# Kernel tuning notes

Measured on AMD Instinct MI355X. Metric: run time of the kernel, lower is better.

The kernel has to match this reference:

```python
import jax, jax.numpy as jnp
import numpy as np
import math

B, L, S = 2, 2048, 2048
DIN, DK, DV, DOUT, H = 512, 512, 512, 512, 8
HEAD_SIZE = DK / H  # attention_head_size = dim_key_query_all / num_attention_heads


def setup_inputs() -> dict:
    key = jax.random.key(0)
    ks = jax.random.split(key, 12)
    inv = 1.0 / math.sqrt(DIN)
    return {
        "queries": jax.random.normal(ks[0], (B, L, DIN), jnp.float32),
        "keys": jax.random.normal(ks[1], (B, S, DIN), jnp.float32),
        "values": jax.random.normal(ks[2], (B, S, DIN), jnp.float32),
        "attn_mask": 0,
        "Wq": jax.random.uniform(ks[3], (DK, DIN), jnp.float32, -inv, inv),
        "Wk": jax.random.uniform(ks[4], (DK, DIN), jnp.float32, -inv, inv),
        "Wv": jax.random.uniform(ks[5], (DV, DIN), jnp.float32, -inv, inv),
        "bv": jax.random.uniform(ks[6], (DV,), jnp.float32, -inv, inv),
        "Wcb": jax.random.uniform(ks[7], (H, DIN), jnp.float32, -inv, inv),
        "mixing": 0.2 * jax.random.normal(ks[8], (H, DK), jnp.float32),
        "Wd": jax.random.uniform(ks[9], (DOUT, DV), jnp.float32, -1.0 / math.sqrt(DV), 1.0 / math.sqrt(DV)),
        "bd": jax.random.uniform(ks[10], (DOUT,), jnp.float32, -1.0 / math.sqrt(DV), 1.0 / math.sqrt(DV)),
    }


def reference(queries, keys, values, attn_mask, Wq, Wk, Wv, bv, Wcb, mixing, Wd, bd):
    # projections
    q = jnp.einsum('bld,ed->ble', queries, Wq)            # [B,L,DK]
    k = jnp.einsum('bsd,ed->bse', keys, Wk)               # [B,S,DK]
    v = jnp.einsum('bsd,ed->bse', values, Wv) + bv        # [B,S,DV]
    v = v.reshape(B, S, H, DV // H).transpose(0, 2, 1, 3)  # [B,H,S,dv]
    # collaborative scores: (q * mixing_h) @ k^T, per head
    mixed_q = q[:, None, :, :] * mixing[None, :, None, :]  # [B,H,L,DK]
    scores = jnp.einsum('bhle,bse->bhls', mixed_q, k)      # [B,H,L,S]
    # content bias: keys -> [B,S,H] -> broadcast over queries
    cb = jnp.einsum('bsd,hd->bhs', keys, Wcb)              # [B,H,S]
    scores = (scores + cb[:, :, None, :]) / math.sqrt(HEAD_SIZE)
    probs = jax.nn.softmax(scores, axis=-1)                # dropout p=0 (eval)
    ctx = jnp.einsum('bhls,bhsv->bhlv', probs, v)          # [B,H,L,dv]
    ctx = ctx.transpose(0, 2, 1, 3).reshape(B, L, DV)      # [B,L,DV]
    out = jnp.einsum('blv,ov->blo', ctx, Wd) + bd          # [B,L,DOUT]
    return out, probs
```

## Files before the change

### kernel.cpp

```cpp
#include <hip/hip_runtime.h>

typedef unsigned short u16;
typedef __bf16 bf16x8 __attribute__((ext_vector_type(8)));
typedef float floatx4 __attribute__((ext_vector_type(4)));

#define B_ 2
#define L_ 2048
#define S_ 2048
#define D_ 512
#define H_ 8

static __device__ __forceinline__ u16 f2bf(float f) {
  union { float f; unsigned u; } v; v.f = f;
  unsigned u = v.u;
  return (u16)((u + 0x7FFFu + ((u >> 16) & 1u)) >> 16);
}
static __device__ __forceinline__ float bf2f(u16 h) {
  union { unsigned u; float f; } v; v.u = ((unsigned)h) << 16;
  return v.f;
}

__global__ __launch_bounds__(256) void qkv_gemm(
    const float* __restrict__ Qin, const float* __restrict__ Kin, const float* __restrict__ Vin,
    const float* __restrict__ Wq, const float* __restrict__ Wk, const float* __restrict__ Wv,
    const float* __restrict__ bv,
    u16* __restrict__ qo, u16* __restrict__ ko, u16* __restrict__ vo)
{
  __shared__ u16 As[128][72];
  __shared__ u16 Bs[128][72];
  const int z = blockIdx.z;
  const float* A = (z == 0) ? Qin : (z == 1) ? Kin : Vin;
  const float* W = (z == 0) ? Wq : (z == 1) ? Wk : Wv;
  const int tid = threadIdx.x;
  const int m0 = blockIdx.y * 128;
  const int n0 = blockIdx.x * 128;
  const int lane = tid & 63, w = tid >> 6;
  const int ml = lane & 15, kl = lane >> 4;
  const int mqw = (w >> 1) * 64, nq = (w & 1) * 64;
  const int srow = tid >> 4, scg = tid & 15;

  floatx4 acc[4][4] = {};

  for (int k0 = 0; k0 < 512; k0 += 64) {
#pragma unroll
    for (int i = 0; i < 8; ++i) {
      const int r = srow + i * 16;
      float4 av = *(const float4*)&A[(size_t)(m0 + r) * 512 + k0 + scg * 4];
      ushort4 ua; ua.x = f2bf(av.x); ua.y = f2bf(av.y); ua.z = f2bf(av.z); ua.w = f2bf(av.w);
      *(ushort4*)&As[r][scg * 4] = ua;
      float4 wv = *(const float4*)&W[(size_t)(n0 + r) * 512 + k0 + scg * 4];
      ushort4 uw; uw.x = f2bf(wv.x); uw.y = f2bf(wv.y); uw.z = f2bf(wv.z); uw.w = f2bf(wv.w);
      *(ushort4*)&Bs[r][scg * 4] = uw;
    }
    __syncthreads();
#pragma unroll
    for (int kk = 0; kk < 64; kk += 32) {
      bf16x8 af[4], bfv[4];
#pragma unroll
      for (int i = 0; i < 4; ++i) af[i] = *(const bf16x8*)&As[mqw + i * 16 + ml][kk + kl * 8];
#pragma unroll
      for (int j = 0; j < 4; ++j) bfv[j] = *(const bf16x8*)&Bs[nq + j * 16 + ml][kk + kl * 8];
#pragma unroll
      for (int i = 0; i < 4; ++i)
#pragma unroll
        for (int j = 0; j < 4; ++j)
          acc[i][j] = __builtin_amdgcn_mfma_f32_16x16x32_bf16(af[i], bfv[j], acc[i][j], 0, 0, 0);
    }
    __syncthreads();
  }
#pragma unroll
  for (int i = 0; i < 4; ++i)
#pragma unroll
    for (int j = 0; j < 4; ++j) {
      const int gc = n0 + nq + j * 16 + ml;
#pragma unroll
      for (int r = 0; r < 4; ++r) {
        const int gr = m0 + mqw + i * 16 + kl * 4 + r;
        float v = acc[i][j][r];
        if (z == 0)      qo[(size_t)gr * 512 + gc] = f2bf(v);
        else if (z == 1) ko[(size_t)gr * 512 + gc] = f2bf(v);
        else             vo[(size_t)gr * 512 + gc] = f2bf(v + bv[gc]);
      }
    }
}

__global__ __launch_bounds__(256) void mixq_kernel(
    const u16* __restrict__ qb, const float* __restrict__ mixing, u16* __restrict__ mq)
{
  __shared__ float mixs[8 * 512];
  const int tid = threadIdx.x;
#pragma unroll
  for (int i = 0; i < 4; ++i)
    *(float4*)&mixs[(tid + i * 256) * 4] = *(const float4*)&mixing[(tid + i * 256) * 4];
  __syncthreads();
  const size_t unit = (size_t)blockIdx.x * 256 + tid;
  const size_t el = unit * 8;
  const int e = (int)(el & 511);
  const size_t bl = el >> 9;
  const int b = (int)(bl >> 11);
  const int l = (int)(bl & 2047);
  uint4 qv = *(const uint4*)&qb[el];
  const float q0 = bf2f((u16)(qv.x & 0xFFFFu)), q1 = bf2f((u16)(qv.x >> 16));
  const float q2 = bf2f((u16)(qv.y & 0xFFFFu)), q3 = bf2f((u16)(qv.y >> 16));
  const float q4 = bf2f((u16)(qv.z & 0xFFFFu)), q5 = bf2f((u16)(qv.z >> 16));
  const float q6 = bf2f((u16)(qv.w & 0xFFFFu)), q7 = bf2f((u16)(qv.w >> 16));
#pragma unroll
  for (int h = 0; h < 8; ++h) {
    const float* mp = &mixs[h * 512 + e];
    uint4 o;
    o.x = (unsigned)f2bf(q0 * mp[0]) | ((unsigned)f2bf(q1 * mp[1]) << 16);
    o.y = (unsigned)f2bf(q2 * mp[2]) | ((unsigned)f2bf(q3 * mp[3]) << 16);
    o.z = (unsigned)f2bf(q4 * mp[4]) | ((unsigned)f2bf(q5 * mp[5]) << 16);
    o.w = (unsigned)f2bf(q6 * mp[6]) | ((unsigned)f2bf(q7 * mp[7]) << 16);
    *(uint4*)&mq[(((size_t)b * 8 + h) * 2048 + l) * 512 + e] = o;
  }
}

__global__ __launch_bounds__(256) void out_gemm(
    const float* __restrict__ A, const float* __restrict__ W,
    const float* __restrict__ bias, float* __restrict__ out)
{
  __shared__ u16 As[128][72];
  __shared__ u16 Bs[128][72];
  const int tid = threadIdx.x;
  const int m0 = blockIdx.y * 128;
  const int n0 = blockIdx.x * 128;
  const int lane = tid & 63, w = tid >> 6;
  const int ml = lane & 15, kl = lane >> 4;
  const int mqw = (w >> 1) * 64, nq = (w & 1) * 64;
  const int srow = tid >> 4, scg = tid & 15;

  floatx4 acc[4][4] = {};

  for (int k0 = 0; k0 < 512; k0 += 64) {
#pragma unroll
    for (int i = 0; i < 8; ++i) {
      const int r = srow + i * 16;
      float4 av = *(const float4*)&A[(size_t)(m0 + r) * 512 + k0 + scg * 4];
      ushort4 ua; ua.x = f2bf(av.x); ua.y = f2bf(av.y); ua.z = f2bf(av.z); ua.w = f2bf(av.w);
      *(ushort4*)&As[r][scg * 4] = ua;
      float4 wv = *(const float4*)&W[(size_t)(n0 + r) * 512 + k0 + scg * 4];
      ushort4 uw; uw.x = f2bf(wv.x); uw.y = f2bf(wv.y); uw.z = f2bf(wv.z); uw.w = f2bf(wv.w);
      *(ushort4*)&Bs[r][scg * 4] = uw;
    }
    __syncthreads();
#pragma unroll
    for (int kk = 0; kk < 64; kk += 32) {
      bf16x8 af[4], bfv[4];
#pragma unroll
      for (int i = 0; i < 4; ++i) af[i] = *(const bf16x8*)&As[mqw + i * 16 + ml][kk + kl * 8];
#pragma unroll
      for (int j = 0; j < 4; ++j) bfv[j] = *(const bf16x8*)&Bs[nq + j * 16 + ml][kk + kl * 8];
#pragma unroll
      for (int i = 0; i < 4; ++i)
#pragma unroll
        for (int j = 0; j < 4; ++j)
          acc[i][j] = __builtin_amdgcn_mfma_f32_16x16x32_bf16(af[i], bfv[j], acc[i][j], 0, 0, 0);
    }
    __syncthreads();
  }
#pragma unroll
  for (int i = 0; i < 4; ++i)
#pragma unroll
    for (int j = 0; j < 4; ++j) {
      const int gc = n0 + nq + j * 16 + ml;
#pragma unroll
      for (int r = 0; r < 4; ++r) {
        const int gr = m0 + mqw + i * 16 + kl * 4 + r;
        out[(size_t)gr * 512 + gc] = acc[i][j][r] + bias[gc];
      }
    }
}

__global__ __launch_bounds__(256) void cb_kernel(
    const float* __restrict__ keys, const float* __restrict__ Wcb, float* __restrict__ cbuf)
{
  __shared__ float Wl[8 * 512];
  const int tid = threadIdx.x;
#pragma unroll
  for (int i = 0; i < 4; ++i) {
    const int idx = tid + i * 256;
    *(float4*)&Wl[idx * 4] = *(const float4*)&Wcb[idx * 4];
  }
  __syncthreads();
  const int w = tid >> 6, lane = tid & 63;
  const int rowid = blockIdx.x * 4 + w;
  const int b = rowid >> 11, s = rowid & 2047;
  const float* kr = keys + (size_t)rowid * 512;
  float acc[8] = {0.f, 0.f, 0.f, 0.f, 0.f, 0.f, 0.f, 0.f};
  for (int e = lane; e < 512; e += 64) {
    const float kv = kr[e];
#pragma unroll
    for (int hh = 0; hh < 8; ++hh) acc[hh] += kv * Wl[hh * 512 + e];
  }
#pragma unroll
  for (int hh = 0; hh < 8; ++hh) {
#pragma unroll
    for (int off = 32; off > 0; off >>= 1) acc[hh] += __shfl_xor(acc[hh], off, 64);
  }
  if (lane == 0) {
#pragma unroll
    for (int hh = 0; hh < 8; ++hh)
      cbuf[((size_t)b * 8 + hh) * 2048 + s] = acc[hh];
  }
}

__global__ __launch_bounds__(256) void transpose_v(
    const u16* __restrict__ vb, u16* __restrict__ vT)
{
  __shared__ u16 t[64][72];
  const int tid = threadIdx.x;
  const int e0 = blockIdx.x * 64;
  const int s0 = blockIdx.y * 64;
  const int b = blockIdx.z;
  const int rr = tid >> 3, g = tid & 7;
#pragma unroll
  for (int i = 0; i < 2; ++i) {
    const int r = rr + i * 32;
    *(uint4*)&t[r][g * 8] = *(const uint4*)&vb[((size_t)b * S_ + s0 + r) * 512 + e0 + g * 8];
  }
  __syncthreads();
#pragma unroll
  for (int i = 0; i < 2; ++i) {
    const int er = rr + i * 32;
    uint4 o;
    o.x = (unsigned)t[g * 8 + 0][er] | ((unsigned)t[g * 8 + 1][er] << 16);
    o.y = (unsigned)t[g * 8 + 2][er] | ((unsigned)t[g * 8 + 3][er] << 16);
    o.z = (unsigned)t[g * 8 + 4][er] | ((unsigned)t[g * 8 + 5][er] << 16);
    o.w = (unsigned)t[g * 8 + 6][er] | ((unsigned)t[g * 8 + 7][er] << 16);
    *(uint4*)&vT[((size_t)b * 512 + e0 + er) * S_ + s0 + g * 8] = o;
  }
}

__global__ __launch_bounds__(256) void scores_gemm(
    const u16* __restrict__ mq, const u16* __restrict__ kb,
    const float* __restrict__ cbuf, float* __restrict__ sc)
{
  __shared__ u16 As[128][72];
  __shared__ u16 Bs[128][72];
  const int tid = threadIdx.x;
  const int bh = blockIdx.z, b = bh >> 3;
  const int m0 = blockIdx.y * 128;
  const int n0 = blockIdx.x * 128;
  const u16* mqb = mq + (size_t)bh * L_ * 512;
  const u16* kbb = kb + (size_t)b * S_ * 512;
  const int lane = tid & 63, w = tid >> 6;
  const int ml = lane & 15, kl = lane >> 4;
  const int mqw = (w >> 1) * 64, nq = (w & 1) * 64;
  const int brow = tid >> 3, bcg = tid & 7;

  floatx4 acc[4][4] = {};

  for (int k0 = 0; k0 < 512; k0 += 64) {
#pragma unroll
    for (int i = 0; i < 4; ++i) {
      const int r = brow + i * 32;
      *(uint4*)&As[r][bcg * 8] = *(const uint4*)&mqb[(size_t)(m0 + r) * 512 + k0 + bcg * 8];
      *(uint4*)&Bs[r][bcg * 8] = *(const uint4*)&kbb[(size_t)(n0 + r) * 512 + k0 + bcg * 8];
    }
    __syncthreads();
#pragma unroll
    for (int kk = 0; kk < 64; kk += 32) {
      bf16x8 af[4], bfv[4];
#pragma unroll
      for (int i = 0; i < 4; ++i) af[i] = *(const bf16x8*)&As[mqw + i * 16 + ml][kk + kl * 8];
#pragma unroll
      for (int j = 0; j < 4; ++j) bfv[j] = *(const bf16x8*)&Bs[nq + j * 16 + ml][kk + kl * 8];
#pragma unroll
      for (int i = 0; i < 4; ++i)
#pragma unroll
        for (int j = 0; j < 4; ++j)
          acc[i][j] = __builtin_amdgcn_mfma_f32_16x16x32_bf16(af[i], bfv[j], acc[i][j], 0, 0, 0);
    }
    __syncthreads();
  }
  float* outp = sc + ((size_t)bh * L_ + m0) * S_ + n0;
#pragma unroll
  for (int j = 0; j < 4; ++j) {
    const int gcl = nq + j * 16 + ml;
    const float cbv = cbuf[(size_t)bh * S_ + n0 + gcl];
#pragma unroll
    for (int i = 0; i < 4; ++i)
#pragma unroll
      for (int r = 0; r < 4; ++r) {
        const int grl = mqw + i * 16 + kl * 4 + r;
        outp[(size_t)grl * S_ + gcl] = (acc[i][j][r] + cbv) * 0.125f;
      }
  }
}

__global__ __launch_bounds__(256) void softmax_ctx(
    float* __restrict__ sc, const u16* __restrict__ vT, float* __restrict__ ctx)
{
  __shared__ u16 Ps[16][1032];
  const int tid = threadIdx.x;
  const int bh = blockIdx.y, b = bh >> 3, h = bh & 7;
  const int l0 = blockIdx.x * 16;
  float* Sg = sc + ((size_t)bh * L_ + l0) * S_;
  const int row = tid >> 4, jg = tid & 15;

  unsigned pr[64];
  float mx = -3.0e38f;
#pragma unroll
  for (int i = 0; i < 32; ++i) {
    const int c = jg * 4 + i * 64;
    float4 v = *(const float4*)&Sg[(size_t)row * S_ + c];
    pr[2 * i]     = (unsigned)f2bf(v.x) | ((unsigned)f2bf(v.y) << 16);
    pr[2 * i + 1] = (unsigned)f2bf(v.z) | ((unsigned)f2bf(v.w) << 16);
    mx = fmaxf(mx, fmaxf(fmaxf(v.x, v.y), fmaxf(v.z, v.w)));
  }
#pragma unroll
  for (int off = 8; off > 0; off >>= 1) mx = fmaxf(mx, __shfl_xor(mx, off, 64));
  float ls = 0.f;
#pragma unroll
  for (int i = 0; i < 64; ++i) {
    const unsigned u = pr[i];
    ls += __expf(bf2f((u16)(u & 0xFFFFu)) - mx) + __expf(bf2f((u16)(u >> 16)) - mx);
  }
#pragma unroll
  for (int off = 8; off > 0; off >>= 1) ls += __shfl_xor(ls, off, 64);
  const float rl = 1.0f / ls;

  const int lane = tid & 63, wv = tid >> 6;
  const int ml = lane & 15, kl = lane >> 4;
  const u16* vrow = vT + ((size_t)b * 512 + h * 64 + wv * 16 + ml) * S_ + kl * 8;
  floatx4 acc = {};

#pragma unroll
  for (int half = 0; half < 2; ++half) {
    __syncthreads();
#pragma unroll
    for (int i = 0; i < 16; ++i) {
      const int ig = i + half * 16;
      const unsigned u0 = pr[2 * ig], u1 = pr[2 * ig + 1];
      float4 p;
      p.x = __expf(bf2f((u16)(u0 & 0xFFFFu)) - mx) * rl;
      p.y = __expf(bf2f((u16)(u0 >> 16)) - mx) * rl;
      p.z = __expf(bf2f((u16)(u1 & 0xFFFFu)) - mx) * rl;
      p.w = __expf(bf2f((u16)(u1 >> 16)) - mx) * rl;
      const int lc = jg * 4 + i * 64;
      *(float4*)&Sg[(size_t)row * S_ + half * 1024 + lc] = p;
      uint2 t;
      t.x = (unsigned)f2bf(p.x) | ((unsigned)f2bf(p.y) << 16);
      t.y = (unsigned)f2bf(p.z) | ((unsigned)f2bf(p.w) << 16);
      *(uint2*)&Ps[row][lc] = t;
    }
    __syncthreads();
    const u16* vk = vrow + half * 1024;
#pragma unroll
    for (int k0 = 0; k0 < 1024; k0 += 32) {
      bf16x8 a  = *(const bf16x8*)&Ps[ml][k0 + kl * 8];
      bf16x8 bb = *(const bf16x8*)&vk[k0];
      acc = __builtin_amdgcn_mfma_f32_16x16x32_bf16(a, bb, acc, 0, 0, 0);
    }
  }
#pragma unroll
  for (int r = 0; r < 4; ++r)
    ctx[((size_t)b * L_ + l0 + kl * 4 + r) * 512 + h * 64 + wv * 16 + ml] = acc[r];
}

extern "C" void kernel_launch(void* const* d_in, const int* in_sizes, int n_in,
                              void* d_out, int out_size, void* d_ws, size_t ws_size,
                              hipStream_t stream) {
  const float* queries = (const float*)d_in[0];
  const float* keys    = (const float*)d_in[1];
  const float* values  = (const float*)d_in[2];
  const float* Wq  = (const float*)d_in[4];
  const float* Wk  = (const float*)d_in[5];
  const float* Wv  = (const float*)d_in[6];
  const float* bv  = (const float*)d_in[7];
  const float* Wcb = (const float*)d_in[8];
  const float* mixing = (const float*)d_in[9];
  const float* Wd  = (const float*)d_in[10];
  const float* bd  = (const float*)d_in[11];

  float* out   = (float*)d_out;
  float* probs = out + (size_t)B_ * L_ * 512;

  char* ws = (char*)d_ws;
  u16*   qb  = (u16*)(ws);
  u16*   kb  = (u16*)(ws + (size_t)4  * 1024 * 1024);
  u16*   vb  = (u16*)(ws + (size_t)8  * 1024 * 1024);
  u16*   vT  = (u16*)(ws + (size_t)12 * 1024 * 1024);
  float* cbuf= (float*)(ws + (size_t)16 * 1024 * 1024);
  float* ctx = (float*)(ws + (size_t)17 * 1024 * 1024);
  u16*   mq  = (u16*)(ws + (size_t)25 * 1024 * 1024);

  hipLaunchKernelGGL(qkv_gemm, dim3(4, 32, 3), dim3(256), 0, stream,
                     queries, keys, values, Wq, Wk, Wv, bv, qb, kb, vb);
  hipLaunchKernelGGL(mixq_kernel, dim3(1024), dim3(256), 0, stream, qb, mixing, mq);
  hipLaunchKernelGGL(cb_kernel, dim3(1024), dim3(256), 0, stream, keys, Wcb, cbuf);
  hipLaunchKernelGGL(transpose_v, dim3(8, 32, 2), dim3(256), 0, stream, vb, vT);
  hipLaunchKernelGGL(scores_gemm, dim3(16, 16, 16), dim3(256), 0, stream,
                     mq, kb, cbuf, probs);
  hipLaunchKernelGGL(softmax_ctx, dim3(128, 16), dim3(256), 0, stream,
                     probs, vT, ctx);
  hipLaunchKernelGGL(out_gemm, dim3(4, 32, 1), dim3(256), 0, stream,
                     ctx, Wd, bd, out);
}
```

Baseline: 677.0 us.

## Fuse scores GEMM with softmax and PV into one attention kernel

Merges the separate scores GEMM and the softmax+context kernel into a single kernel. Each block computes a 16-row strip of scores directly from registers with MFMA, keeps them packed as bf16, reduces the row max and sum across waves through shared memory, and writes the probs once. This removes the fp32 scores write and the re-read of the full score matrix. In exchange, K tiles are loaded straight from global memory with no LDS reuse across row tiles, so K traffic grows since each block re-reads all K rows for its batch.

```diff
diff --git a/kernel.cpp b/kernel.cpp
--- a/kernel.cpp
+++ b/kernel.cpp
@@ -232,118 +232,127 @@
   }
 }
 
-__global__ __launch_bounds__(256) void scores_gemm(
+__global__ __launch_bounds__(256, 2) void fused_attn(
     const u16* __restrict__ mq, const u16* __restrict__ kb,
-    const float* __restrict__ cbuf, float* __restrict__ sc)
-{
-  __shared__ u16 As[128][72];
-  __shared__ u16 Bs[128][72];
-  const int tid = threadIdx.x;
-  const int bh = blockIdx.z, b = bh >> 3;
-  const int m0 = blockIdx.y * 128;
-  const int n0 = blockIdx.x * 128;
-  const u16* mqb = mq + (size_t)bh * L_ * 512;
-  const u16* kbb = kb + (size_t)b * S_ * 512;
+    const float* __restrict__ cbuf, const u16* __restrict__ vT,
+    float* __restrict__ probs, float* __restrict__ ctx)
+{
+  __shared__ u16 Ps[16][1032];
+  __shared__ float redm[16][4];
+  __shared__ float reds[16][4];
+  const int tid = threadIdx.x;
+  const int bh = blockIdx.y, b = bh >> 3, h = bh & 7;
+  const int l0 = blockIdx.x * 16;
   const int lane = tid & 63, w = tid >> 6;
   const int ml = lane & 15, kl = lane >> 4;
-  const int mqw = (w >> 1) * 64, nq = (w & 1) * 64;
-  const int brow = tid >> 3, bcg = tid & 7;
-
-  floatx4 acc[4][4] = {};
-
-  for (int k0 = 0; k0 < 512; k0 += 64) {
-#pragma unroll
-    for (int i = 0; i < 4; ++i) {
-      const int r = brow + i * 32;
-      *(uint4*)&As[r][bcg * 8] = *(const uint4*)&mqb[(size_t)(m0 + r) * 512 + k0 + bcg * 8];
-      *(uint4*)&Bs[r][bcg * 8] = *(const uint4*)&kbb[(size_t)(n0 + r) * 512 + k0 + bcg * 8];
-    }
-    __syncthreads();
-#pragma unroll
-    for (int kk = 0; kk < 64; kk += 32) {
-      bf16x8 af[4], bfv[4];
-#pragma unroll
-      for (int i = 0; i < 4; ++i) af[i] = *(const bf16x8*)&As[mqw + i * 16 + ml][kk + kl * 8];
-#pragma unroll
-      for (int j = 0; j < 4; ++j) bfv[j] = *(const bf16x8*)&Bs[nq + j * 16 + ml][kk + kl * 8];
-#pragma unroll
-      for (int i = 0; i < 4; ++i)
-#pragma unroll
-        for (int j = 0; j < 4; ++j)
-          acc[i][j] = __builtin_amdgcn_mfma_f32_16x16x32_bf16(af[i], bfv[j], acc[i][j], 0, 0, 0);
-    }
-    __syncthreads();
-  }
-  float* outp = sc + ((size_t)bh * L_ + m0) * S_ + n0;
-#pragma unroll
-  for (int j = 0; j < 4; ++j) {
-    const int gcl = nq + j * 16 + ml;
-    const float cbv = cbuf[(size_t)bh * S_ + n0 + gcl];
-#pragma unroll
-    for (int i = 0; i < 4; ++i)
-#pragma unroll
-      for (int r = 0; r < 4; ++r) {
-        const int grl = mqw + i * 16 + kl * 4 + r;
-        outp[(size_t)grl * S_ + gcl] = (acc[i][j][r] + cbv) * 0.125f;
+  const int n0w = w * 512;
+
+  const u16* arow = mq + ((size_t)bh * L_ + l0 + ml) * 512 + kl * 8;
+  bf16x8 af[16];
+#pragma unroll
+  for (int ks = 0; ks < 16; ++ks)
+    af[ks] = *(const bf16x8*)(arow + ks * 32);
+
+  const u16* kbb = kb + (size_t)b * S_ * 512;
+  const float* cbp = cbuf + (size_t)bh * S_;
+
+  unsigned pr[64];
+  float mx[4] = {-3.0e38f, -3.0e38f, -3.0e38f, -3.0e38f};
+#pragma unroll
+  for (int t = 0; t < 32; ++t) {
+    const u16* brow = kbb + (size_t)(n0w + t * 16 + ml) * 512 + kl * 8;
+    floatx4 acc = {};
+#pragma unroll
+    for (int ks = 0; ks < 16; ++ks) {
+      bf16x8 bfv = *(const bf16x8*)(brow + ks * 32);
+      acc = __builtin_amdgcn_mfma_f32_16x16x32_bf16(af[ks], bfv, acc, 0, 0, 0);
+    }
+    const float cbv = cbp[n0w + t * 16 + ml];
+    float s0 = (acc[0] + cbv) * 0.125f;
+    float s1 = (acc[1] + cbv) * 0.125f;
+    float s2 = (acc[2] + cbv) * 0.125f;
+    float s3 = (acc[3] + cbv) * 0.125f;
+    mx[0] = fmaxf(mx[0], s0); mx[1] = fmaxf(mx[1], s1);
+    mx[2] = fmaxf(mx[2], s2); mx[3] = fmaxf(mx[3], s3);
+    pr[2 * t]     = (unsigned)f2bf(s0) | ((unsigned)f2bf(s1) << 16);
+    pr[2 * t + 1] = (unsigned)f2bf(s2) | ((unsigned)f2bf(s3) << 16);
+  }
+
+#pragma unroll
+  for (int r = 0; r < 4; ++r)
+#pragma unroll
+    for (int off = 1; off < 16; off <<= 1)
+      mx[r] = fmaxf(mx[r], __shfl_xor(mx[r], off, 64));
+  if (ml == 0) {
+#pragma unroll
+    for (int r = 0; r < 4; ++r) redm[kl * 4 + r][w] = mx[r];
+  }
+  __syncthreads();
+#pragma unroll
+  for (int r = 0; r < 4; ++r) {
+    const float* rm = redm[kl * 4 + r];
+    mx[r] = fmaxf(fmaxf(rm[0], rm[1]), fmaxf(rm[2], rm[3]));
+  }
+
+  float ls[4] = {0.f, 0.f, 0.f, 0.f};
+#pragma unroll
+  for (int t = 0; t < 32; ++t) {
+    const unsigned u0 = pr[2 * t], u1 = pr[2 * t + 1];
+    ls[0] += __expf(bf2f((u16)(u0 & 0xFFFFu)) - mx[0]);
+    ls[1] += __expf(bf2f((u16)(u0 >> 16))     - mx[1]);
+    ls[2] += __expf(bf2f((u16)(u1 & 0xFFFFu)) - mx[2]);
+    ls[3] += __expf(bf2f((u16)(u1 >> 16))     - mx[3]);
+  }
+#pragma unroll
+  for (int r = 0; r < 4; ++r)
+#pragma unroll
+    for (int off = 1; off < 16; off <<= 1)
+      ls[r] += __shfl_xor(ls[r], off, 64);
+  if (ml == 0) {
+#pragma unroll
+    for (int r = 0; r < 4; ++r) reds[kl * 4 + r][w] = ls[r];
+  }
+  __syncthreads();
+  float rl[4];
+#pragma unroll
+  for (int r = 0; r < 4; ++r) {
+    const float* rs = reds[kl * 4 + r];
+    rl[r] = 1.0f / (rs[0] + rs[1] + rs[2] + rs[3]);
+  }
+
+  float* Pg = probs + ((size_t)bh * L_ + l0) * S_;
+#pragma unroll
+  for (int t = 0; t < 32; ++t) {
+    const int col = n0w + t * 16 + ml;
+    const unsigned u0 = pr[2 * t], u1 = pr[2 * t + 1];
+    float p0 = __expf(bf2f((u16)(u0 & 0xFFFFu)) - mx[0]) * rl[0];
+    float p1 = __expf(bf2f((u16)(u0 >> 16))     - mx[1]) * rl[1];
+    float p2 = __expf(bf2f((u16)(u1 & 0xFFFFu)) - mx[2]) * rl[2];
+    float p3 = __expf(bf2f((u16)(u1 >> 16))     - mx[3]) * rl[3];
+    Pg[(size_t)(kl * 4 + 0) * S_ + col] = p0;
+    Pg[(size_t)(kl * 4 + 1) * S_ + col] = p1;
+    Pg[(size_t)(kl * 4 + 2) * S_ + col] = p2;
+    Pg[(size_t)(kl * 4 + 3) * S_ + col] = p3;
+    pr[2 * t]     = (unsigned)f2bf(p0) | ((unsigned)f2bf(p1) << 16);
+    pr[2 * t + 1] = (unsigned)f2bf(p2) | ((unsigned)f2bf(p3) << 16);
+  }
+
+  floatx4 acc = {};
+  const u16* vrow = vT + ((size_t)b * 512 + h * 64 + w * 16 + ml) * (size_t)S_ + kl * 8;
+#pragma unroll
+  for (int half = 0; half < 2; ++half) {
+    __syncthreads();
+    if ((w >> 1) == half) {
+      const int cbase = (w & 1) * 512;
+#pragma unroll
+      for (int t = 0; t < 32; ++t) {
+        const int col = cbase + t * 16 + ml;
+        const unsigned u0 = pr[2 * t], u1 = pr[2 * t + 1];
+        Ps[kl * 4 + 0][col] = (u16)(u0 & 0xFFFFu);
+        Ps[kl * 4 + 1][col] = (u16)(u0 >> 16);
+        Ps[kl * 4 + 2][col] = (u16)(u1 & 0xFFFFu);
+        Ps[kl * 4 + 3][col] = (u16)(u1 >> 16);
       }
-  }
-}
-
-__global__ __launch_bounds__(256) void softmax_ctx(
-    float* __restrict__ sc, const u16* __restrict__ vT, float* __restrict__ ctx)
-{
-  __shared__ u16 Ps[16][1032];
-  const int tid = threadIdx.x;
-  const int bh = blockIdx.y, b = bh >> 3, h = bh & 7;
-  const int l0 = blockIdx.x * 16;
-  float* Sg = sc + ((size_t)bh * L_ + l0) * S_;
-  const int row = tid >> 4, jg = tid & 15;
-
-  unsigned pr[64];
-  float mx = -3.0e38f;
-#pragma unroll
-  for (int i = 0; i < 32; ++i) {
-    const int c = jg * 4 + i * 64;
-    float4 v = *(const float4*)&Sg[(size_t)row * S_ + c];
-    pr[2 * i]     = (unsigned)f2bf(v.x) | ((unsigned)f2bf(v.y) << 16);
-    pr[2 * i + 1] = (unsigned)f2bf(v.z) | ((unsigned)f2bf(v.w) << 16);
-    mx = fmaxf(mx, fmaxf(fmaxf(v.x, v.y), fmaxf(v.z, v.w)));
-  }
-#pragma unroll
-  for (int off = 8; off > 0; off >>= 1) mx = fmaxf(mx, __shfl_xor(mx, off, 64));
-  float ls = 0.f;
-#pragma unroll
-  for (int i = 0; i < 64; ++i) {
-    const unsigned u = pr[i];
-    ls += __expf(bf2f((u16)(u & 0xFFFFu)) - mx) + __expf(bf2f((u16)(u >> 16)) - mx);
-  }
-#pragma unroll
-  for (int off = 8; off > 0; off >>= 1) ls += __shfl_xor(ls, off, 64);
-  const float rl = 1.0f / ls;
-
-  const int lane = tid & 63, wv = tid >> 6;
-  const int ml = lane & 15, kl = lane >> 4;
-  const u16* vrow = vT + ((size_t)b * 512 + h * 64 + wv * 16 + ml) * S_ + kl * 8;
-  floatx4 acc = {};
-
-#pragma unroll
-  for (int half = 0; half < 2; ++half) {
-    __syncthreads();
-#pragma unroll
-    for (int i = 0; i < 16; ++i) {
-      const int ig = i + half * 16;
-      const unsigned u0 = pr[2 * ig], u1 = pr[2 * ig + 1];
-      float4 p;
-      p.x = __expf(bf2f((u16)(u0 & 0xFFFFu)) - mx) * rl;
-      p.y = __expf(bf2f((u16)(u0 >> 16)) - mx) * rl;
-      p.z = __expf(bf2f((u16)(u1 & 0xFFFFu)) - mx) * rl;
-      p.w = __expf(bf2f((u16)(u1 >> 16)) - mx) * rl;
-      const int lc = jg * 4 + i * 64;
-      *(float4*)&Sg[(size_t)row * S_ + half * 1024 + lc] = p;
-      uint2 t;
-      t.x = (unsigned)f2bf(p.x) | ((unsigned)f2bf(p.y) << 16);
-      t.y = (unsigned)f2bf(p.z) | ((unsigned)f2bf(p.w) << 16);
-      *(uint2*)&Ps[row][lc] = t;
     }
     __syncthreads();
     const u16* vk = vrow + half * 1024;
@@ -356,7 +365,7 @@
   }
 #pragma unroll
   for (int r = 0; r < 4; ++r)
-    ctx[((size_t)b * L_ + l0 + kl * 4 + r) * 512 + h * 64 + wv * 16 + ml] = acc[r];
+    ctx[((size_t)b * L_ + l0 + kl * 4 + r) * 512 + h * 64 + w * 16 + ml] = acc[r];
 }
 
 extern "C" void kernel_launch(void* const* d_in, const int* in_sizes, int n_in,
@@ -391,10 +400,8 @@
   hipLaunchKernelGGL(mixq_kernel, dim3(1024), dim3(256), 0, stream, qb, mixing, mq);
   hipLaunchKernelGGL(cb_kernel, dim3(1024), dim3(256), 0, stream, keys, Wcb, cbuf);
   hipLaunchKernelGGL(transpose_v, dim3(8, 32, 2), dim3(256), 0, stream, vb, vT);
-  hipLaunchKernelGGL(scores_gemm, dim3(16, 16, 16), dim3(256), 0, stream,
-                     mq, kb, cbuf, probs);
-  hipLaunchKernelGGL(softmax_ctx, dim3(128, 16), dim3(256), 0, stream,
-                     probs, vT, ctx);
+  hipLaunchKernelGGL(fused_attn, dim3(128, 16), dim3(256), 0, stream,
+                     mq, kb, cbuf, vT, probs, ctx);
   hipLaunchKernelGGL(out_gemm, dim3(4, 32, 1), dim3(256), 0, stream,
                      ctx, Wd, bd, out);
 }
```

After: 945.8 us. 39.7% more time.
